# Kernel tuning notes

Hardware: AMD Instinct MI355X
Metric: run time of the kernel (lower is better)

## Reference

```python
import jax, jax.numpy as jnp
import numpy as np

N, D, C, S, E, K, MIN_MATCH, N_ITER = 100000, 128, 16, 16, 3200000, 64, 1, 4


def setup_inputs() -> dict:
    key = jax.random.key(0)
    k1, k2, k3, k4 = jax.random.split(key, 4)
    es = jax.random.normal(k1, (N, D), jnp.float32)
    edge_index = jax.random.randint(k2, (2, E), 0, N)
    seeds = jax.random.randint(k3, (C, S), 0, N)
    W = jax.random.normal(k4, (D, D), jnp.float32) / np.float32(np.sqrt(D))
    return {"es": es, "edge_index": edge_index, "seeds": seeds, "W": W, "n_iter": N_ITER}


def _memory_step(es, idx, hx, W):
    # ragged gather of last expansion, padded to fixed size per class: [C, k, D]
    inp = es[idx]
    d = inp.shape[-1]
    q = jnp.mean(inp, axis=1) if hx is None else hx          # attention query [C, D]
    logits = jnp.einsum('ckd,cd->ck', inp, q) / jnp.sqrt(jnp.float32(d))
    a = jax.nn.softmax(logits, axis=-1)                      # [C, k]
    ctx = jnp.einsum('ck,ckd->cd', a, inp)                   # attended read [C, D]
    pre = ctx if hx is None else ctx + hx                    # recurrent memory update
    return jnp.tanh(pre @ W)                                 # [C, D]


def _cosine(x, y):
    xn = x / (jnp.linalg.norm(x, axis=-1, keepdims=True) + 1e-8)
    yn = y / (jnp.linalg.norm(y, axis=-1, keepdims=True) + 1e-8)
    return xn @ yn.T                                         # [N, C]


def _expand(es, W, edge_index, seeds, n_iter):
    n, c = es.shape[0], seeds.shape[0]
    src, dst = edge_index[0], edge_index[1]
    # known_mask.scatter_(0, seed_all, 1)
    known = jnp.zeros((n,), bool).at[seeds.ravel()].set(True)
    # get_cate_mask(seeds, N): per-class membership mask [C, N]
    cate = jnp.zeros((c, n), bool).at[jnp.arange(c)[:, None], seeds].set(True)
    hx, last = None, seeds
    outs, exps, hxes = [], [], []
    for _ in range(n_iter):
        hx = _memory_step(es, last, hx, W)
        # get_cate_neighbors: per-class count of in-edges whose source is in the class
        counts = jax.vmap(lambda m: jax.ops.segment_sum(m, dst, num_segments=n))(
            cate.astype(jnp.float32)[:, src])                # [C, N]
        valid = (counts >= MIN_MATCH) & (~known)[None, :]    # [C, N]
        scores = _cosine(es, hx).T                           # [C, N]
        # _select: top n_expansion valid nodes per class (finite fill avoids -inf grads)
        probs, idx = jax.lax.top_k(jnp.where(valid, scores, -1e9), K)
        known = known.at[idx.ravel()].set(True)
        cate = cate.at[jnp.arange(c)[:, None], idx].set(True)
        last = idx
        outs.append(probs); exps.append(idx); hxes.append(hx)
    return jnp.stack(outs), jnp.stack(exps), jnp.stack(hxes)


def reference(es, edge_index, seeds, W, n_iter):
    return _expand(es, W, edge_index, seeds, n_iter)
```

## Files before the change

### kernel.cpp

```cpp
#include <hip/hip_runtime.h>
#include <math.h>

#define NN 100000
#define DD 128
#define CC 16
#define SS 16
#define EE 3200000
#define KK 64
#define NIT 4
#define CNT_STRIDE 32
#define NB 32
#define SLMAX 4096
#define MM (NB * KK)
#define EB ((EE + 255) / 256)
#define INF_STAMP 0x7fffffff

typedef unsigned long long ull;

__device__ inline ull ordkey(double d) {
    long long b = __double_as_longlong(d);
    return (b < 0) ? ~(ull)b : ((ull)b | 0x8000000000000000ULL);
}
__device__ inline double keyord(ull u) {
    long long b = (u & 0x8000000000000000ULL)
                    ? (long long)(u & 0x7FFFFFFFFFFFFFFFULL)
                    : (long long)~u;
    return __longlong_as_double(b);
}
__device__ inline bool gt(ull ka, int na, ull kb, int nb) {
    return (ka > kb) || (ka == kb && na < nb);
}

__device__ inline void wsort64(ull& k, int& n, int lane) {
    for (int k2 = 2; k2 <= 64; k2 <<= 1) {
        for (int j = k2 >> 1; j; j >>= 1) {
            ull ok = __shfl_xor(k, j, 64);
            int on = __shfl_xor(n, j, 64);
            bool isLow = (lane & j) == 0;
            bool d = (k2 == 64) || ((lane & k2) == 0);
            bool wantMax = (d == isLow);
            if (wantMax == gt(ok, on, k, n)) { k = ok; n = on; }
        }
    }
}
__device__ inline void wmerge64(ull& k, int& n, int lane) {
    for (int j = 32; j; j >>= 1) {
        ull ok = __shfl_xor(k, j, 64);
        int on = __shfl_xor(n, j, 64);
        bool wantMax = (lane & j) == 0;
        if (wantMax == gt(ok, on, k, n)) { k = ok; n = on; }
    }
}


__global__ __launch_bounds__(256)
void k_init(const float* __restrict__ es, double* __restrict__ inv_norm,
            int* __restrict__ known, unsigned* __restrict__ cate,
            unsigned* __restrict__ nbr) {
    int wave = threadIdx.x >> 6, lane = threadIdx.x & 63;
    int n = blockIdx.x * 4 + wave;
    if (n >= NN) return;
    float a = es[(long)n * DD + lane];
    float b = es[(long)n * DD + 64 + lane];
    double p = (double)a * (double)a + (double)b * (double)b;
    for (int o = 32; o > 0; o >>= 1) p += __shfl_xor(p, o, 64);
    if (lane == 0) {
        inv_norm[n] = 1.0 / (sqrt(p) + 1e-8);
        known[n] = INF_STAMP;
        cate[n] = 0;
        nbr[n] = 0;
    }
}

__global__ void k_seed(const int* __restrict__ seeds, int* __restrict__ known,
                       unsigned* __restrict__ cate) {
    int i = threadIdx.x;
    if (i < CC * SS) {
        int n = seeds[i];
        known[n] = 0;
        atomicOr(&cate[n], 1u << (i / SS));
    }
}


__global__ __launch_bounds__(256)
void k_memedge(const float* __restrict__ es, const float* __restrict__ Wm,
               const int* __restrict__ seeds, const int* __restrict__ last,
               double* __restrict__ hx, double* __restrict__ hxn,
               float* __restrict__ out, int* __restrict__ cnt,
               const int* __restrict__ edge, const unsigned* __restrict__ cate,
               unsigned* __restrict__ nbr, int t) {
    __shared__ float  inp[KK][DD + 1];
    __shared__ int    rowS[KK];
    __shared__ double q[DD];
    __shared__ double lg[KK];
    __shared__ double sr[KK];
    __shared__ double pre[DD];
    __shared__ double red[DD];
    int tid = threadIdx.x;

    if (blockIdx.x >= CC) {
        long e = (long)(blockIdx.x - CC) * 256 + tid;
        if (e < EE) {
            int s = edge[e];
            unsigned m = cate[s];
            if (m) {
                int d = edge[EE + e];
                atomicOr(&nbr[d], m);
            }
        }
        return;
    }

    int c = blockIdx.x;
    if (tid == 0) cnt[c * CNT_STRIDE] = 0;
    int k = (t == 0) ? SS : KK;
    if (tid < KK) {
        lg[tid] = -1.0e308;
        if (tid < k) rowS[tid] = (t == 0) ? seeds[c * SS + tid] : last[c * KK + tid];
    }
    __syncthreads();
    for (int i = tid; i < k * DD; i += 256)
        inp[i >> 7][i & 127] = es[(long)rowS[i >> 7] * DD + (i & 127)];
    __syncthreads();
    if (tid < DD) {
        if (t == 0) {
            double s = 0;
            for (int j = 0; j < k; ++j) s += (double)inp[j][tid];
            q[tid] = s / (double)k;
        } else {
            q[tid] = hx[c * DD + tid];
        }
    }
    __syncthreads();
    if (tid < k) {
        double s = 0;
        for (int i = 0; i < DD; ++i) s += (double)inp[tid][i] * q[i];
        lg[tid] = s / sqrt((double)DD);
    }
    __syncthreads();
    if (tid < KK) sr[tid] = lg[tid];
    __syncthreads();
    for (int st = 32; st > 0; st >>= 1) {
        if (tid < st) sr[tid] = fmax(sr[tid], sr[tid + st]);
        __syncthreads();
    }
    double mx = sr[0];
    __syncthreads();
    if (tid < KK) {
        double e = (tid < k) ? exp(lg[tid] - mx) : 0.0;
        lg[tid] = e; sr[tid] = e;
    }
    __syncthreads();
    for (int st = 32; st > 0; st >>= 1) {
        if (tid < st) sr[tid] += sr[tid + st];
        __syncthreads();
    }
    double sm = sr[0];
    __syncthreads();
    if (tid < KK) lg[tid] /= sm;
    __syncthreads();
    if (tid < DD) {
        double ctx = 0;
        for (int j = 0; j < k; ++j) ctx += lg[j] * (double)inp[j][tid];
        pre[tid] = (t == 0) ? ctx : (ctx + q[tid]);
    }
    __syncthreads();
    double h = 0;
    if (tid < DD) {
        for (int i = 0; i < DD; ++i) h += pre[i] * (double)Wm[i * DD + tid];
        h = tanh(h);
        red[tid] = h * h;
    }
    __syncthreads();
    for (int st = 64; st > 0; st >>= 1) {
        if (tid < st) red[tid] += red[tid + st];
        __syncthreads();
    }
    if (tid < DD) {
        double inv = 1.0 / (sqrt(red[0]) + 1e-8);
        hx[c * DD + tid] = h;
        hxn[c * DD + tid] = h * inv;
        out[2 * NIT * CC * KK + t * CC * DD + c * DD + tid] = (float)h;
    }
}


__global__ __launch_bounds__(256)
void k_cand(const float* __restrict__ es, const double* __restrict__ inv_norm,
            const int* __restrict__ known, const unsigned* __restrict__ nbr,
            const double* __restrict__ hxn,
            int* __restrict__ cnt, int* __restrict__ cidx,
            ull* __restrict__ ckey, int cap, int t) {
    __shared__ int    pair[256 * 16];
    __shared__ short  prank[256 * 16];
    __shared__ double hxnL[CC * 129];
    __shared__ int    lcnt[CC];
    __shared__ int    base[CC];
    __shared__ int    npair;
    int tid = threadIdx.x;

    for (int i = tid; i < CC * DD; i += 256)
        hxnL[(i >> 7) * 129 + (i & 127)] = hxn[i];
    if (tid < CC) lcnt[tid] = 0;
    if (tid == 0) npair = 0;
    __syncthreads();

    int n = blockIdx.x * 256 + tid;
    unsigned m = 0;
    if (n < NN && known[n] > t) m = nbr[n];
    while (m) {
        int c = __ffs(m) - 1;
        m &= m - 1;
        int r = atomicAdd(&lcnt[c], 1);
        int p = atomicAdd(&npair, 1);
        pair[p] = (n << 4) | c;
        prank[p] = (short)r;
    }
    __syncthreads();

    if (tid < CC && lcnt[tid] > 0)
        base[tid] = atomicAdd(&cnt[tid * CNT_STRIDE], lcnt[tid]);
    __syncthreads();

    int np = npair;
    for (int t2 = tid; t2 < np; t2 += 256) {
        int pk = pair[t2];
        int nn = pk >> 4, c = pk & 15;
        const float4* row = (const float4*)(es + (long)nn * DD);
        const double* h = &hxnL[c * 129];
        double s = 0;
        #pragma unroll
        for (int i = 0; i < 32; ++i) {
            float4 v = row[i];
            s += (double)v.x * h[4 * i + 0] + (double)v.y * h[4 * i + 1]
               + (double)v.z * h[4 * i + 2] + (double)v.w * h[4 * i + 3];
        }
        int pos = base[c] + (int)prank[t2];
        if (pos < cap) {
            cidx[(long)c * cap + pos] = nn;
            ckey[(long)c * cap + pos] = ordkey(s * inv_norm[nn]);
        }
    }
}


__global__ __launch_bounds__(256)
void k_top(const int* __restrict__ cnt, const int* __restrict__ cidx,
           const ull* __restrict__ ckey, int cap,
           ull* __restrict__ tkey, int* __restrict__ tnode) {
    __shared__ ull ks[SLMAX];
    __shared__ int ns[SLMAX];
    int c = blockIdx.x / NB, b = blockIdx.x % NB;
    int tid = threadIdx.x, wave = tid >> 6, lane = tid & 63;
    int count = min(cnt[c * CNT_STRIDE], cap);
    int per = (count + NB - 1) / NB;
    int start = b * per;
    int m = min(per, count - start);
    int sl = 64;
    while (sl < per) sl <<= 1;
    int nruns = sl >> 6;
    for (int r = wave; r < nruns; r += 4) {
        int i = (r << 6) + lane;
        ull k; int n;
        if (i < m) { k = ckey[(long)c * cap + start + i]; n = cidx[(long)c * cap + start + i]; }
        else       { k = 0ULL; n = 0x7FFFFFFF; }
        wsort64(k, n, lane);
        ks[i] = k; ns[i] = n;
    }
    __syncthreads();
    for (int step = 1; step < nruns; step <<= 1) {
        int npair2 = nruns / (2 * step);
        for (int pr = wave; pr < npair2; pr += 4) {
            int ra = pr * 2 * step, rb = ra + step;
            ull ka = ks[(ra << 6) + lane];       int na = ns[(ra << 6) + lane];
            ull kb = ks[(rb << 6) + 63 - lane];  int nb2 = ns[(rb << 6) + 63 - lane];
            if (gt(kb, nb2, ka, na)) { ka = kb; na = nb2; }
            wmerge64(ka, na, lane);
            ks[(ra << 6) + lane] = ka; ns[(ra << 6) + lane] = na;
        }
        __syncthreads();
    }
    if (tid < KK) {
        tkey[(long)c * MM + b * KK + tid] = ks[tid];
        tnode[(long)c * MM + b * KK + tid] = ns[tid];
    }
}


__global__ __launch_bounds__(256)
void k_mergeupd(const int* __restrict__ cnt,
                const ull* __restrict__ tkey, const int* __restrict__ tnode,
                int* __restrict__ known, const unsigned* __restrict__ nbr,
                unsigned* __restrict__ cate, int* __restrict__ last,
                float* __restrict__ out, int cap, int t) {
    __shared__ ull ks[MM];
    __shared__ int ns[MM];
    int c = blockIdx.x, tid = threadIdx.x, wave = tid >> 6, lane = tid & 63;
    for (int i = tid; i < MM; i += 256) {
        ks[i] = tkey[(long)c * MM + i];
        ns[i] = tnode[(long)c * MM + i];
    }
    __syncthreads();
    for (int step = 1; step < NB; step <<= 1) {
        int npair2 = NB / (2 * step);
        for (int pr = wave; pr < npair2; pr += 4) {
            int ra = pr * 2 * step, rb = ra + step;
            ull ka = ks[(ra << 6) + lane];       int na = ns[(ra << 6) + lane];
            ull kb = ks[(rb << 6) + 63 - lane];  int nb2 = ns[(rb << 6) + 63 - lane];
            if (gt(kb, nb2, ka, na)) { ka = kb; na = nb2; }
            wmerge64(ka, na, lane);
            ks[(ra << 6) + lane] = ka; ns[(ra << 6) + lane] = na;
        }
        __syncthreads();
    }
    int count = min(cnt[c * CNT_STRIDE], cap);
    int nsel = min(count, KK);
    if (tid < KK && tid < nsel) {
        int n = ns[tid];
        out[t * CC * KK + c * KK + tid] = (float)keyord(ks[tid]);
        out[NIT * CC * KK + t * CC * KK + c * KK + tid] = (float)n;
        last[c * KK + tid] = n;
        known[n] = t + 1;
        atomicOr(&cate[n], 1u << c);
    }
    if (tid == 0 && nsel < KK) {
        int r = nsel;
        for (int n = 0; n < NN && r < KK; ++n) {
            bool valid = ((nbr[n] >> c) & 1u) && (known[n] > t);
            if (!valid) {
                out[t * CC * KK + c * KK + r] = -1e9f;
                out[NIT * CC * KK + t * CC * KK + c * KK + r] = (float)n;
                last[c * KK + r] = n;
                known[n] = t + 1;
                atomicOr(&cate[n], 1u << c);
                ++r;
            }
        }
    }
}


extern "C" void kernel_launch(void* const* d_in, const int* in_sizes, int n_in,
                              void* d_out, int out_size, void* d_ws, size_t ws_size,
                              hipStream_t stream) {
    const float* es    = (const float*)d_in[0];
    const int*   edge  = (const int*)d_in[1];
    const int*   seeds = (const int*)d_in[2];
    const float* W     = (const float*)d_in[3];
    float* out = (float*)d_out;

    char* p = (char*)d_ws;
    auto alloc = [&](size_t bytes) -> char* {
        char* r = p;
        p += (bytes + 255) & ~(size_t)255;
        return r;
    };
    double*   inv_norm = (double*)alloc((size_t)NN * 8);
    int*      known    = (int*)alloc((size_t)NN * 4);
    unsigned* cate     = (unsigned*)alloc((size_t)NN * 4);
    unsigned* nbr      = (unsigned*)alloc((size_t)NN * 4);
    double*   hx       = (double*)alloc(CC * DD * 8);
    double*   hxn      = (double*)alloc(CC * DD * 8);
    int*      last     = (int*)alloc(CC * KK * 4);
    int*      cnt      = (int*)alloc(CC * CNT_STRIDE * 4);
    ull*      tkey     = (ull*)alloc((size_t)CC * MM * 8);
    int*      tnode    = (int*)alloc((size_t)CC * MM * 4);
    size_t used = (size_t)(p - (char*)d_ws);
    size_t rem = (ws_size > used + 8192) ? (ws_size - used - 8192) : 0;
    long capl = (long)(rem / (CC * 12));
    if (capl > NN) capl = NN;
    if (capl < 1) capl = 1;
    int cap = (int)capl;
    int*    cidx = (int*)alloc((size_t)CC * cap * 4);
    ull*    ckey = (ull*)alloc((size_t)CC * cap * 8);

    k_init<<<(NN + 3) / 4, 256, 0, stream>>>(es, inv_norm, known, cate, nbr);
    k_seed<<<1, 256, 0, stream>>>(seeds, known, cate);

    for (int t = 0; t < NIT; ++t) {
        k_memedge<<<CC + EB, 256, 0, stream>>>(es, W, seeds, last, hx, hxn, out,
                                               cnt, edge, cate, nbr, t);
        k_cand<<<(NN + 255) / 256, 256, 0, stream>>>(es, inv_norm, known, nbr, hxn,
                                                     cnt, cidx, ckey, cap, t);
        k_top<<<CC * NB, 256, 0, stream>>>(cnt, cidx, ckey, cap, tkey, tnode);
        k_mergeupd<<<CC, 256, 0, stream>>>(cnt, tkey, tnode, known, nbr,
                                           cate, last, out, cap, t);
    }
}
```

Before: 310.3 us.

## Drop norm precompute, fuse seed init, grid-stride edge pass

```diff
diff --git a/kernel.cpp b/kernel.cpp
--- a/kernel.cpp
+++ b/kernel.cpp
@@ -12,7 +12,7 @@
 #define NB 32
 #define SLMAX 4096
 #define MM (NB * KK)
-#define EB ((EE + 255) / 256)
+#define EBLK 2048
 #define INF_STAMP 0x7fffffff
 
 typedef unsigned long long ull;
@@ -54,31 +54,24 @@
 
 
 __global__ __launch_bounds__(256)
-void k_init(const float* __restrict__ es, double* __restrict__ inv_norm,
-            int* __restrict__ known, unsigned* __restrict__ cate,
-            unsigned* __restrict__ nbr) {
-    int wave = threadIdx.x >> 6, lane = threadIdx.x & 63;
+void k_init(const int* __restrict__ seeds, int* __restrict__ known,
+            unsigned* __restrict__ cate, unsigned* __restrict__ nbr) {
+    __shared__ int sd[CC * SS];
+    int tid = threadIdx.x;
+    if (tid < CC * SS) sd[tid] = seeds[tid];
+    __syncthreads();
+    int wave = tid >> 6, lane = tid & 63;
     int n = blockIdx.x * 4 + wave;
     if (n >= NN) return;
-    float a = es[(long)n * DD + lane];
-    float b = es[(long)n * DD + 64 + lane];
-    double p = (double)a * (double)a + (double)b * (double)b;
-    for (int o = 32; o > 0; o >>= 1) p += __shfl_xor(p, o, 64);
+    unsigned m = 0;
+    #pragma unroll
+    for (int e = lane; e < CC * SS; e += 64)
+        if (sd[e] == n) m |= 1u << (e / SS);
+    for (int o = 32; o > 0; o >>= 1) m |= __shfl_xor(m, o, 64);
     if (lane == 0) {
-        inv_norm[n] = 1.0 / (sqrt(p) + 1e-8);
-        known[n] = INF_STAMP;
-        cate[n] = 0;
+        known[n] = m ? 0 : INF_STAMP;
+        cate[n] = m;
         nbr[n] = 0;
-    }
-}
-
-__global__ void k_seed(const int* __restrict__ seeds, int* __restrict__ known,
-                       unsigned* __restrict__ cate) {
-    int i = threadIdx.x;
-    if (i < CC * SS) {
-        int n = seeds[i];
-        known[n] = 0;
-        atomicOr(&cate[n], 1u << (i / SS));
     }
 }
 
@@ -100,14 +93,11 @@
     int tid = threadIdx.x;
 
     if (blockIdx.x >= CC) {
-        long e = (long)(blockIdx.x - CC) * 256 + tid;
-        if (e < EE) {
+        for (long e = (long)(blockIdx.x - CC) * 256 + tid; e < EE;
+             e += (long)EBLK * 256) {
             int s = edge[e];
             unsigned m = cate[s];
-            if (m) {
-                int d = edge[EE + e];
-                atomicOr(&nbr[d], m);
-            }
+            if (m) atomicOr(&nbr[edge[EE + e]], m);
         }
         return;
     }
@@ -187,7 +177,7 @@
 
 
 __global__ __launch_bounds__(256)
-void k_cand(const float* __restrict__ es, const double* __restrict__ inv_norm,
+void k_cand(const float* __restrict__ es,
             const int* __restrict__ known, const unsigned* __restrict__ nbr,
             const double* __restrict__ hxn,
             int* __restrict__ cnt, int* __restrict__ cidx,
@@ -229,17 +219,19 @@
         int nn = pk >> 4, c = pk & 15;
         const float4* row = (const float4*)(es + (long)nn * DD);
         const double* h = &hxnL[c * 129];
-        double s = 0;
+        double s = 0, p2 = 0;
         #pragma unroll
         for (int i = 0; i < 32; ++i) {
             float4 v = row[i];
-            s += (double)v.x * h[4 * i + 0] + (double)v.y * h[4 * i + 1]
-               + (double)v.z * h[4 * i + 2] + (double)v.w * h[4 * i + 3];
+            double vx = v.x, vy = v.y, vz = v.z, vw = v.w;
+            s  += vx * h[4 * i + 0] + vy * h[4 * i + 1]
+                + vz * h[4 * i + 2] + vw * h[4 * i + 3];
+            p2 += vx * vx + vy * vy + vz * vz + vw * vw;
         }
         int pos = base[c] + (int)prank[t2];
         if (pos < cap) {
             cidx[(long)c * cap + pos] = nn;
-            ckey[(long)c * cap + pos] = ordkey(s * inv_norm[nn]);
+            ckey[(long)c * cap + pos] = ordkey(s / (sqrt(p2) + 1e-8));
         }
     }
 }
@@ -356,7 +348,6 @@
         p += (bytes + 255) & ~(size_t)255;
         return r;
     };
-    double*   inv_norm = (double*)alloc((size_t)NN * 8);
     int*      known    = (int*)alloc((size_t)NN * 4);
     unsigned* cate     = (unsigned*)alloc((size_t)NN * 4);
     unsigned* nbr      = (unsigned*)alloc((size_t)NN * 4);
@@ -375,13 +366,12 @@
     int*    cidx = (int*)alloc((size_t)CC * cap * 4);
     ull*    ckey = (ull*)alloc((size_t)CC * cap * 8);
 
-    k_init<<<(NN + 3) / 4, 256, 0, stream>>>(es, inv_norm, known, cate, nbr);
-    k_seed<<<1, 256, 0, stream>>>(seeds, known, cate);
+    k_init<<<(NN + 3) / 4, 256, 0, stream>>>(seeds, known, cate, nbr);
 
     for (int t = 0; t < NIT; ++t) {
-        k_memedge<<<CC + EB, 256, 0, stream>>>(es, W, seeds, last, hx, hxn, out,
-                                               cnt, edge, cate, nbr, t);
-        k_cand<<<(NN + 255) / 256, 256, 0, stream>>>(es, inv_norm, known, nbr, hxn,
+        k_memedge<<<CC + EBLK, 256, 0, stream>>>(es, W, seeds, last, hx, hxn, out,
+                                                 cnt, edge, cate, nbr, t);
+        k_cand<<<(NN + 255) / 256, 256, 0, stream>>>(es, known, nbr, hxn,
                                                      cnt, cidx, ckey, cap, t);
         k_top<<<CC * NB, 256, 0, stream>>>(cnt, cidx, ckey, cap, tkey, tnode);
         k_mergeupd<<<CC, 256, 0, stream>>>(cnt, tkey, tnode, known, nbr,
```

Measured after the change: 303.9 us. -2.1%, faster.
